# Optimization experiments

Measured on AMD Instinct MI355X. Metric: run time of the kernel, lower is better.

## Reference

```python
import jax, jax.numpy as jnp
import numpy as np

BOUND = 5.0
MIN_D = 1e-3
MIN_BW = 1e-3
MIN_BH = 1e-3
EPS = 1e-8
B, F, K = 131072, 256, 16


def setup_inputs() -> dict:
    key = jax.random.key(0)
    k1, k2, k3, k4 = jax.random.split(key, 4)
    return {
        "x": jax.random.normal(k1, (B, F), dtype=jnp.float32),
        "uw": jax.random.normal(k2, (F, K), dtype=jnp.float32),
        "uh": jax.random.normal(k3, (F, K), dtype=jnp.float32),
        "ud": jax.random.normal(k4, (F, K - 1), dtype=jnp.float32),
        "input_shift": jnp.zeros((F,), dtype=jnp.float32),
        "input_scale": jnp.ones((F,), dtype=jnp.float32),
    }


def _knots(u, mb):
    # u: [F, K] unnormalized bin sizes -> knot positions [F, K+1] and sizes [F, K]
    f, k = u.shape
    w = jax.nn.softmax(u, axis=-1)
    w = mb + (1.0 - mb * k) * w
    c = jnp.concatenate([jnp.zeros((f, 1), u.dtype), jnp.cumsum(w, axis=-1)], axis=-1)
    c = 2.0 * BOUND * c - BOUND
    c = c.at[:, 0].set(-BOUND).at[:, -1].set(BOUND)
    return c, c[:, 1:] - c[:, :-1]


def reference(x, uw, uh, ud, input_shift, input_scale):
    f, k = uw.shape
    # normalize input to spline domain
    xn = (x - input_shift[None, :]) / input_scale[None, :]

    # knot positions / bin sizes
    cw, w = _knots(uw, MIN_BW)   # [F, K+1], [F, K]
    ch, h = _knots(uh, MIN_BH)

    # derivatives at knots; boundaries padded so derivative = 1 (linear tails)
    const = float(np.log(np.expm1(1.0 - MIN_D)))
    pad = jnp.full((f, 1), const, dtype=ud.dtype)
    d = MIN_D + jax.nn.softplus(jnp.concatenate([pad, ud, pad], axis=-1))  # [F, K+1]

    inside = (xn > -BOUND) & (xn < BOUND)
    xc = jnp.clip(xn, -BOUND, BOUND)

    # per-feature bucketize: searchsorted over each feature's knots
    idx = jax.vmap(lambda a, v: jnp.searchsorted(a, v, side="right"),
                   in_axes=(0, 1), out_axes=1)(cw, xc) - 1  # [B, F]
    idx = jnp.clip(idx, 0, k - 1)

    fa = jnp.arange(f)[None, :]
    icw = cw[fa, idx]   # left knot x
    ibw = w[fa, idx]    # bin width
    ich = ch[fa, idx]   # left knot y
    ibh = h[fa, idx]    # bin height
    delta = ibh / ibw
    d0 = d[fa, idx]
    d1 = d[fa, idx + 1]

    # rational-quadratic evaluation
    theta = (xc - icw) / ibw
    t1m = theta * (1.0 - theta)
    numer = ibh * (delta * theta * theta + d0 * t1m)
    denom = delta + (d0 + d1 - 2.0 * delta) * t1m
    s = jnp.where(inside, ich + numer / denom, xn)  # identity linear tails

    # gauge fix: standardize per feature with batch stats (biased var)
    mean = jnp.mean(s, axis=0)
    var = jnp.mean((s - mean[None, :]) ** 2, axis=0)
    z = (s - mean[None, :]) / jnp.sqrt(var[None, :] + EPS)
    return z
```

## Files before the change

### kernel.cpp

```cpp
#include <hip/hip_runtime.h>
#include <math.h>


#define FEAT 256
#define KBINS 16
#define BATCH 131072
#define BOUNDF 5.0f
#define MIN_Df 1e-3f
#define MIN_BWf 1e-3f
#define MIN_BHf 1e-3f
#define EPSF 1e-8f

#define FT_TILES 4
#define FT 64
#define RB 256
#define ROWS_PB (BATCH / RB)
#define SLOTS 4
#define ITERS (ROWS_PB / SLOTS)

#define OFF_P0   0
#define OFF_P1   17408
#define OFF_CW   34816
#define OFF_MEAN 39168
#define OFF_ISTD 39424
#define OFF_PS   39680
#define OFF_PS2  (OFF_PS + 1024 * 64)

__global__ __launch_bounds__(256) void k_params(const float* __restrict__ uw,
                                                const float* __restrict__ uh,
                                                const float* __restrict__ ud,
                                                float* __restrict__ ws) {
    int f = threadIdx.x;
    float cw[17], ch[17], dv[17];
    {
        float u[KBINS];
#pragma unroll
        for (int j = 0; j < KBINS; j++) u[j] = uw[f * KBINS + j];
        float m = u[0];
#pragma unroll
        for (int j = 1; j < KBINS; j++) m = fmaxf(m, u[j]);
        float ssum = 0.f;
#pragma unroll
        for (int j = 0; j < KBINS; j++) { u[j] = expf(u[j] - m); ssum += u[j]; }
        float inv = 1.0f / ssum;
        float cum = 0.f;
        cw[0] = -BOUNDF;
#pragma unroll
        for (int j = 1; j < KBINS; j++) {
            float wj = MIN_BWf + (1.0f - MIN_BWf * (float)KBINS) * (u[j - 1] * inv);
            cum += wj;
            cw[j] = 2.0f * BOUNDF * cum - BOUNDF;
        }
        cw[KBINS] = BOUNDF;
    }
    {
        float u[KBINS];
#pragma unroll
        for (int j = 0; j < KBINS; j++) u[j] = uh[f * KBINS + j];
        float m = u[0];
#pragma unroll
        for (int j = 1; j < KBINS; j++) m = fmaxf(m, u[j]);
        float ssum = 0.f;
#pragma unroll
        for (int j = 0; j < KBINS; j++) { u[j] = expf(u[j] - m); ssum += u[j]; }
        float inv = 1.0f / ssum;
        float cum = 0.f;
        ch[0] = -BOUNDF;
#pragma unroll
        for (int j = 1; j < KBINS; j++) {
            float wj = MIN_BHf + (1.0f - MIN_BHf * (float)KBINS) * (u[j - 1] * inv);
            cum += wj;
            ch[j] = 2.0f * BOUNDF * cum - BOUNDF;
        }
        ch[KBINS] = BOUNDF;
    }
    {
        dv[0] = 1.0f;
        dv[KBINS] = 1.0f;
#pragma unroll
        for (int j = 1; j < KBINS; j++) {
            float v = ud[f * (KBINS - 1) + (j - 1)];
            float sp = fmaxf(v, 0.0f) + log1pf(expf(-fabsf(v)));
            dv[j] = MIN_Df + sp;
        }
    }
#pragma unroll
    for (int j = 0; j <= KBINS; j++) ws[OFF_CW + f * 17 + j] = cw[j];
    float4* P0g = (float4*)(ws + OFF_P0);
    float4* P1g = (float4*)(ws + OFF_P1);
#pragma unroll
    for (int i = 0; i < KBINS; i++) {
        float w = cw[i + 1] - cw[i];
        float binv = 1.0f / w;
        float hb = ch[i + 1] - ch[i];
        float delta = hb * binv;
        float4 p0, p1;
        p0.x = cw[i] * binv;
        p0.y = binv;
        p0.z = hb * delta;
        p0.w = hb * dv[i];
        p1.x = dv[i] + dv[i + 1] - 2.0f * delta;
        p1.y = delta;
        p1.z = ch[i];
        p1.w = 0.0f;
        P0g[f * 17 + i] = p0;
        P1g[f * 17 + i] = p1;
    }
}

__device__ __forceinline__ float eval_rq(float xv, float a, float nb,
                                         const float4* __restrict__ sP0,
                                         const float4* __restrict__ sP1,
                                         const float kn[15], int l17) {
    float xn = fmaf(xv, a, nb);
    float xc = fminf(fmaxf(xn, -BOUNDF), BOUNDF);
    int idx = 0;
#pragma unroll
    for (int j = 0; j < 15; j++) idx += (xc >= kn[j]) ? 1 : 0;
    int o = l17 + idx;
    float4 p0 = sP0[o];
    float4 p1 = sP1[o];
    float th = fmaf(xc, p0.y, -p0.x);
    float th2 = th * th;
    float t1m = th - th2;
    float numer = fmaf(p0.z, th2, p0.w * t1m);
    float denom = fmaf(p1.x, t1m, p1.y);
    float s = fmaf(numer, __builtin_amdgcn_rcpf(denom), p1.z);
    return (fabsf(xn) < BOUNDF) ? s : xn;
}

__global__ __launch_bounds__(256, 4) void k_pass1(const float* __restrict__ X,
                                                  const float* __restrict__ shiftp,
                                                  const float* __restrict__ scalep,
                                                  float* __restrict__ ws) {
    __shared__ float4 sP0[FT * 17];
    __shared__ float4 sP1[FT * 17];
    __shared__ float red[2][SLOTS][FT];
    int t = threadIdx.x;
    int rb = blockIdx.x, ft = blockIdx.y;
    const float4* P0g = (const float4*)(ws + OFF_P0) + ft * FT * 17;
    const float4* P1g = (const float4*)(ws + OFF_P1) + ft * FT * 17;
    for (int i = t; i < FT * 17; i += 256) { sP0[i] = P0g[i]; sP1[i] = P1g[i]; }
    int l = t & 63, slot = t >> 6;
    int f = ft * FT + l;
    float kn[15];
#pragma unroll
    for (int j = 0; j < 15; j++) kn[j] = ws[OFF_CW + f * 17 + 1 + j];
    float a = 1.0f / scalep[f];
    float nb = -shiftp[f] * a;
    int l17 = l * 17;
    __syncthreads();
    const float* Xp = X + (size_t)(rb * ROWS_PB + slot) * FEAT + f;
    float sum = 0.f, sumsq = 0.f;
    for (int r = 0; r < ITERS; r += 4) {
        float x0 = Xp[0 * SLOTS * FEAT];
        float x1 = Xp[1 * SLOTS * FEAT];
        float x2 = Xp[2 * SLOTS * FEAT];
        float x3 = Xp[3 * SLOTS * FEAT];
        Xp += 4 * SLOTS * FEAT;
        float s0 = eval_rq(x0, a, nb, sP0, sP1, kn, l17);
        float s1 = eval_rq(x1, a, nb, sP0, sP1, kn, l17);
        float s2 = eval_rq(x2, a, nb, sP0, sP1, kn, l17);
        float s3 = eval_rq(x3, a, nb, sP0, sP1, kn, l17);
        sum += s0; sumsq = fmaf(s0, s0, sumsq);
        sum += s1; sumsq = fmaf(s1, s1, sumsq);
        sum += s2; sumsq = fmaf(s2, s2, sumsq);
        sum += s3; sumsq = fmaf(s3, s3, sumsq);
    }
    red[0][slot][l] = sum;
    red[1][slot][l] = sumsq;
    __syncthreads();
    if (t < FT) {
        float v = red[0][0][t] + red[0][1][t] + red[0][2][t] + red[0][3][t];
        ws[OFF_PS + (ft * RB + rb) * FT + t] = v;
    } else if (t < 2 * FT) {
        int u = t - FT;
        float v = red[1][0][u] + red[1][1][u] + red[1][2][u] + red[1][3][u];
        ws[OFF_PS2 + (ft * RB + rb) * FT + u] = v;
    }
}

__global__ __launch_bounds__(256) void k_reduce(float* __restrict__ ws) {
    int f = blockIdx.x;
    int ft = f >> 6, l = f & 63;
    int t = threadIdx.x;
    __shared__ float r1[256], r2[256];
    r1[t] = ws[OFF_PS + (ft * RB + t) * FT + l];
    r2[t] = ws[OFF_PS2 + (ft * RB + t) * FT + l];
    __syncthreads();
    for (int off = 128; off > 0; off >>= 1) {
        if (t < off) { r1[t] += r1[t + off]; r2[t] += r2[t + off]; }
        __syncthreads();
    }
    if (t == 0) {
        float mean = r1[0] * (1.0f / (float)BATCH);
        float var = r2[0] * (1.0f / (float)BATCH) - mean * mean;
        var = fmaxf(var, 0.0f);
        ws[OFF_MEAN + f] = mean;
        ws[OFF_ISTD + f] = 1.0f / sqrtf(var + EPSF);
    }
}

__global__ __launch_bounds__(256, 4) void k_pass2(const float* __restrict__ X,
                                                  const float* __restrict__ shiftp,
                                                  const float* __restrict__ scalep,
                                                  const float* __restrict__ ws,
                                                  float* __restrict__ Z) {
    __shared__ float4 sP0[FT * 17];
    __shared__ float4 sP1[FT * 17];
    int t = threadIdx.x;
    int rb = blockIdx.x, ft = blockIdx.y;
    const float4* P0g = (const float4*)(ws + OFF_P0) + ft * FT * 17;
    const float4* P1g = (const float4*)(ws + OFF_P1) + ft * FT * 17;
    for (int i = t; i < FT * 17; i += 256) { sP0[i] = P0g[i]; sP1[i] = P1g[i]; }
    int l = t & 63, slot = t >> 6;
    int f = ft * FT + l;
    float kn[15];
#pragma unroll
    for (int j = 0; j < 15; j++) kn[j] = ws[OFF_CW + f * 17 + 1 + j];
    float a = 1.0f / scalep[f];
    float nb = -shiftp[f] * a;
    float mean = ws[OFF_MEAN + f];
    float istd = ws[OFF_ISTD + f];
    int l17 = l * 17;
    __syncthreads();
    size_t base = (size_t)(rb * ROWS_PB + slot) * FEAT + f;
    const float* Xp = X + base;
    float* Zp = Z + base;
    for (int r = 0; r < ITERS; r += 4) {
        float x0 = Xp[0 * SLOTS * FEAT];
        float x1 = Xp[1 * SLOTS * FEAT];
        float x2 = Xp[2 * SLOTS * FEAT];
        float x3 = Xp[3 * SLOTS * FEAT];
        Xp += 4 * SLOTS * FEAT;
        float s0 = eval_rq(x0, a, nb, sP0, sP1, kn, l17);
        float s1 = eval_rq(x1, a, nb, sP0, sP1, kn, l17);
        float s2 = eval_rq(x2, a, nb, sP0, sP1, kn, l17);
        float s3 = eval_rq(x3, a, nb, sP0, sP1, kn, l17);
        Zp[0 * SLOTS * FEAT] = (s0 - mean) * istd;
        Zp[1 * SLOTS * FEAT] = (s1 - mean) * istd;
        Zp[2 * SLOTS * FEAT] = (s2 - mean) * istd;
        Zp[3 * SLOTS * FEAT] = (s3 - mean) * istd;
        Zp += 4 * SLOTS * FEAT;
    }
}

extern "C" void kernel_launch(void* const* d_in, const int* in_sizes, int n_in,
                              void* d_out, int out_size, void* d_ws, size_t ws_size,
                              hipStream_t stream) {
    const float* x     = (const float*)d_in[0];
    const float* uw    = (const float*)d_in[1];
    const float* uh    = (const float*)d_in[2];
    const float* ud    = (const float*)d_in[3];
    const float* shift = (const float*)d_in[4];
    const float* scale = (const float*)d_in[5];
    float* out = (float*)d_out;
    float* ws  = (float*)d_ws;

    k_params<<<1, 256, 0, stream>>>(uw, uh, ud, ws);
    k_pass1<<<dim3(RB, FT_TILES), 256, 0, stream>>>(x, shift, scale, ws);
    k_reduce<<<FEAT, 256, 0, stream>>>(ws);
    k_pass2<<<dim3(RB, FT_TILES), 256, 0, stream>>>(x, shift, scale, ws, out);
}
```

Before: 116.8 us.

## Cache spline output as bf16 in pass 1 and stream-normalize in pass 2

Pass 1 now writes the spline output as bf16 into workspace, and a new vectorized pass 2 reads it back and applies the per-feature normalization, replacing the re-read of x and re-evaluation of the spline. Feature tiles shrink to 32 with 8 row slots, and occupancy hints are raised. Total memory traffic stays about the same, but pass 2 drops the searchsorted and rational-quadratic math. This relies on enough workspace (falling back to the old path otherwise) and adds bf16 rounding error to the output.

```diff
diff --git a/kernel.cpp b/kernel.cpp
--- a/kernel.cpp
+++ b/kernel.cpp
@@ -11,25 +11,34 @@
 #define MIN_BHf 1e-3f
 #define EPSF 1e-8f
 
-#define FT_TILES 4
-#define FT 64
-#define RB 256
-#define ROWS_PB (BATCH / RB)
-#define SLOTS 4
-#define ITERS (ROWS_PB / SLOTS)
-
-#define OFF_P0   0
-#define OFF_P1   17408
-#define OFF_CW   34816
-#define OFF_MEAN 39168
-#define OFF_ISTD 39424
-#define OFF_PS   39680
-#define OFF_PS2  (OFF_PS + 1024 * 64)
+#define FTB 32
+#define FT_TILES 8
+#define SLOTB 8
+#define RBB 256
+#define ROWS_PB (BATCH / RBB)
+#define ITERB (ROWS_PB / SLOTB)
+
+#define R_P0   0
+#define R_P1   17408
+#define R_CW   34816
+#define R_MEAN 39168
+#define R_ISTD 39424
+#define R_PS   39680
+#define R_PS2  (R_PS + 2048 * 32)
+#define TAB_FLOATS (R_PS2 + 2048 * 32)
+#define S_ELEMS ((size_t)BATCH * FEAT)
+#define S_FLOATS (S_ELEMS / 2)
+
+__device__ __forceinline__ unsigned short f2bf(float x) {
+    unsigned int b = __float_as_uint(x);
+    unsigned int r = (b + 0x7fffu + ((b >> 16) & 1u)) >> 16;
+    return (unsigned short)r;
+}
 
 __global__ __launch_bounds__(256) void k_params(const float* __restrict__ uw,
                                                 const float* __restrict__ uh,
                                                 const float* __restrict__ ud,
-                                                float* __restrict__ ws) {
+                                                float* __restrict__ tab) {
     int f = threadIdx.x;
     float cw[17], ch[17], dv[17];
     {
@@ -85,9 +94,9 @@
         }
     }
 #pragma unroll
-    for (int j = 0; j <= KBINS; j++) ws[OFF_CW + f * 17 + j] = cw[j];
-    float4* P0g = (float4*)(ws + OFF_P0);
-    float4* P1g = (float4*)(ws + OFF_P1);
+    for (int j = 0; j <= KBINS; j++) tab[R_CW + f * 17 + j] = cw[j];
+    float4* P0g = (float4*)(tab + R_P0);
+    float4* P1g = (float4*)(tab + R_P1);
 #pragma unroll
     for (int i = 0; i < KBINS; i++) {
         float w = cw[i + 1] - cw[i];
@@ -129,39 +138,50 @@
     return (fabsf(xn) < BOUNDF) ? s : xn;
 }
 
-__global__ __launch_bounds__(256, 4) void k_pass1(const float* __restrict__ X,
+template <bool STORE_S>
+__global__ __launch_bounds__(256, 6) void k_pass1(const float* __restrict__ X,
                                                   const float* __restrict__ shiftp,
                                                   const float* __restrict__ scalep,
-                                                  float* __restrict__ ws) {
-    __shared__ float4 sP0[FT * 17];
-    __shared__ float4 sP1[FT * 17];
-    __shared__ float red[2][SLOTS][FT];
+                                                  float* __restrict__ tab,
+                                                  unsigned short* __restrict__ S) {
+    __shared__ float4 sP0[FTB * 17];
+    __shared__ float4 sP1[FTB * 17];
+    __shared__ float red[2][SLOTB][FTB];
     int t = threadIdx.x;
     int rb = blockIdx.x, ft = blockIdx.y;
-    const float4* P0g = (const float4*)(ws + OFF_P0) + ft * FT * 17;
-    const float4* P1g = (const float4*)(ws + OFF_P1) + ft * FT * 17;
-    for (int i = t; i < FT * 17; i += 256) { sP0[i] = P0g[i]; sP1[i] = P1g[i]; }
-    int l = t & 63, slot = t >> 6;
-    int f = ft * FT + l;
+    const float4* P0g = (const float4*)(tab + R_P0) + ft * FTB * 17;
+    const float4* P1g = (const float4*)(tab + R_P1) + ft * FTB * 17;
+    for (int i = t; i < FTB * 17; i += 256) { sP0[i] = P0g[i]; sP1[i] = P1g[i]; }
+    int l = t & 31, slot = t >> 5;
+    int f = ft * FTB + l;
     float kn[15];
 #pragma unroll
-    for (int j = 0; j < 15; j++) kn[j] = ws[OFF_CW + f * 17 + 1 + j];
+    for (int j = 0; j < 15; j++) kn[j] = tab[R_CW + f * 17 + 1 + j];
     float a = 1.0f / scalep[f];
     float nb = -shiftp[f] * a;
     int l17 = l * 17;
     __syncthreads();
-    const float* Xp = X + (size_t)(rb * ROWS_PB + slot) * FEAT + f;
+    size_t base = (size_t)(rb * ROWS_PB + slot) * FEAT + f;
+    const float* Xp = X + base;
+    unsigned short* Sp = STORE_S ? (S + base) : nullptr;
     float sum = 0.f, sumsq = 0.f;
-    for (int r = 0; r < ITERS; r += 4) {
-        float x0 = Xp[0 * SLOTS * FEAT];
-        float x1 = Xp[1 * SLOTS * FEAT];
-        float x2 = Xp[2 * SLOTS * FEAT];
-        float x3 = Xp[3 * SLOTS * FEAT];
-        Xp += 4 * SLOTS * FEAT;
+    for (int r = 0; r < ITERB; r += 4) {
+        float x0 = Xp[0 * SLOTB * FEAT];
+        float x1 = Xp[1 * SLOTB * FEAT];
+        float x2 = Xp[2 * SLOTB * FEAT];
+        float x3 = Xp[3 * SLOTB * FEAT];
+        Xp += 4 * SLOTB * FEAT;
         float s0 = eval_rq(x0, a, nb, sP0, sP1, kn, l17);
         float s1 = eval_rq(x1, a, nb, sP0, sP1, kn, l17);
         float s2 = eval_rq(x2, a, nb, sP0, sP1, kn, l17);
         float s3 = eval_rq(x3, a, nb, sP0, sP1, kn, l17);
+        if (STORE_S) {
+            Sp[0 * SLOTB * FEAT] = f2bf(s0);
+            Sp[1 * SLOTB * FEAT] = f2bf(s1);
+            Sp[2 * SLOTB * FEAT] = f2bf(s2);
+            Sp[3 * SLOTB * FEAT] = f2bf(s3);
+            Sp += 4 * SLOTB * FEAT;
+        }
         sum += s0; sumsq = fmaf(s0, s0, sumsq);
         sum += s1; sumsq = fmaf(s1, s1, sumsq);
         sum += s2; sumsq = fmaf(s2, s2, sumsq);
@@ -170,23 +190,27 @@
     red[0][slot][l] = sum;
     red[1][slot][l] = sumsq;
     __syncthreads();
-    if (t < FT) {
-        float v = red[0][0][t] + red[0][1][t] + red[0][2][t] + red[0][3][t];
-        ws[OFF_PS + (ft * RB + rb) * FT + t] = v;
-    } else if (t < 2 * FT) {
-        int u = t - FT;
-        float v = red[1][0][u] + red[1][1][u] + red[1][2][u] + red[1][3][u];
-        ws[OFF_PS2 + (ft * RB + rb) * FT + u] = v;
-    }
-}
-
-__global__ __launch_bounds__(256) void k_reduce(float* __restrict__ ws) {
+    if (t < FTB) {
+        float v = 0.f;
+#pragma unroll
+        for (int s2i = 0; s2i < SLOTB; s2i++) v += red[0][s2i][t];
+        tab[R_PS + (ft * RBB + rb) * FTB + t] = v;
+    } else if (t < 2 * FTB) {
+        int u = t - FTB;
+        float v = 0.f;
+#pragma unroll
+        for (int s2i = 0; s2i < SLOTB; s2i++) v += red[1][s2i][u];
+        tab[R_PS2 + (ft * RBB + rb) * FTB + u] = v;
+    }
+}
+
+__global__ __launch_bounds__(256) void k_reduce(float* __restrict__ tab) {
     int f = blockIdx.x;
-    int ft = f >> 6, l = f & 63;
+    int ft = f >> 5, l = f & 31;
     int t = threadIdx.x;
     __shared__ float r1[256], r2[256];
-    r1[t] = ws[OFF_PS + (ft * RB + t) * FT + l];
-    r2[t] = ws[OFF_PS2 + (ft * RB + t) * FT + l];
+    r1[t] = tab[R_PS + (ft * RBB + t) * FTB + l];
+    r2[t] = tab[R_PS2 + (ft * RBB + t) * FTB + l];
     __syncthreads();
     for (int off = 128; off > 0; off >>= 1) {
         if (t < off) { r1[t] += r1[t + off]; r2[t] += r2[t + off]; }
@@ -196,52 +220,87 @@
         float mean = r1[0] * (1.0f / (float)BATCH);
         float var = r2[0] * (1.0f / (float)BATCH) - mean * mean;
         var = fmaxf(var, 0.0f);
-        ws[OFF_MEAN + f] = mean;
-        ws[OFF_ISTD + f] = 1.0f / sqrtf(var + EPSF);
-    }
-}
-
-__global__ __launch_bounds__(256, 4) void k_pass2(const float* __restrict__ X,
-                                                  const float* __restrict__ shiftp,
-                                                  const float* __restrict__ scalep,
-                                                  const float* __restrict__ ws,
-                                                  float* __restrict__ Z) {
-    __shared__ float4 sP0[FT * 17];
-    __shared__ float4 sP1[FT * 17];
+        tab[R_MEAN + f] = mean;
+        tab[R_ISTD + f] = 1.0f / sqrtf(var + EPSF);
+    }
+}
+
+__global__ __launch_bounds__(256, 8) void k_pass2_stream(const unsigned short* __restrict__ S,
+                                                         const float* __restrict__ tab,
+                                                         float* __restrict__ Z) {
+    int gid = blockIdx.x * 256 + threadIdx.x;
+    int fg = gid & 31;
+    int rs = gid >> 5;
+    const float* meanp = tab + R_MEAN + fg * 8;
+    const float* istdp = tab + R_ISTD + fg * 8;
+    float istd[8], nmi[8];
+#pragma unroll
+    for (int j = 0; j < 8; j++) {
+        float m = meanp[j];
+        float is = istdp[j];
+        istd[j] = is;
+        nmi[j] = -m * is;
+    }
+    size_t idx = (size_t)rs * 8 * FEAT + fg * 8;
+#pragma unroll
+    for (int r = 0; r < 8; r++) {
+        uint4 sv = *(const uint4*)(S + idx);
+        float z0 = fmaf(__uint_as_float((sv.x & 0xffffu) << 16), istd[0], nmi[0]);
+        float z1 = fmaf(__uint_as_float(sv.x & 0xffff0000u),     istd[1], nmi[1]);
+        float z2 = fmaf(__uint_as_float((sv.y & 0xffffu) << 16), istd[2], nmi[2]);
+        float z3 = fmaf(__uint_as_float(sv.y & 0xffff0000u),     istd[3], nmi[3]);
+        float z4 = fmaf(__uint_as_float((sv.z & 0xffffu) << 16), istd[4], nmi[4]);
+        float z5 = fmaf(__uint_as_float(sv.z & 0xffff0000u),     istd[5], nmi[5]);
+        float z6 = fmaf(__uint_as_float((sv.w & 0xffffu) << 16), istd[6], nmi[6]);
+        float z7 = fmaf(__uint_as_float(sv.w & 0xffff0000u),     istd[7], nmi[7]);
+        float4* Zp = (float4*)(Z + idx);
+        Zp[0] = make_float4(z0, z1, z2, z3);
+        Zp[1] = make_float4(z4, z5, z6, z7);
+        idx += FEAT;
+    }
+}
+
+__global__ __launch_bounds__(256, 6) void k_pass2_eval(const float* __restrict__ X,
+                                                       const float* __restrict__ shiftp,
+                                                       const float* __restrict__ scalep,
+                                                       const float* __restrict__ tab,
+                                                       float* __restrict__ Z) {
+    __shared__ float4 sP0[FTB * 17];
+    __shared__ float4 sP1[FTB * 17];
     int t = threadIdx.x;
     int rb = blockIdx.x, ft = blockIdx.y;
-    const float4* P0g = (const float4*)(ws + OFF_P0) + ft * FT * 17;
-    const float4* P1g = (const float4*)(ws + OFF_P1) + ft * FT * 17;
-    for (int i = t; i < FT * 17; i += 256) { sP0[i] = P0g[i]; sP1[i] = P1g[i]; }
-    int l = t & 63, slot = t >> 6;
-    int f = ft * FT + l;
+    const float4* P0g = (const float4*)(tab + R_P0) + ft * FTB * 17;
+    const float4* P1g = (const float4*)(tab + R_P1) + ft * FTB * 17;
+    for (int i = t; i < FTB * 17; i += 256) { sP0[i] = P0g[i]; sP1[i] = P1g[i]; }
+    int l = t & 31, slot = t >> 5;
+    int f = ft * FTB + l;
     float kn[15];
 #pragma unroll
-    for (int j = 0; j < 15; j++) kn[j] = ws[OFF_CW + f * 17 + 1 + j];
+    for (int j = 0; j < 15; j++) kn[j] = tab[R_CW + f * 17 + 1 + j];
     float a = 1.0f / scalep[f];
     float nb = -shiftp[f] * a;
-    float mean = ws[OFF_MEAN + f];
-    float istd = ws[OFF_ISTD + f];
+    float mean = tab[R_MEAN + f];
+    float istd = tab[R_ISTD + f];
     int l17 = l * 17;
     __syncthreads();
     size_t base = (size_t)(rb * ROWS_PB + slot) * FEAT + f;
     const float* Xp = X + base;
     float* Zp = Z + base;
-    for (int r = 0; r < ITERS; r += 4) {
-        float x0 = Xp[0 * SLOTS * FEAT];
-        float x1 = Xp[1 * SLOTS * FEAT];
-        float x2 = Xp[2 * SLOTS * FEAT];
-        float x3 = Xp[3 * SLOTS * FEAT];
-        Xp += 4 * SLOTS * FEAT;
+    for (int r = 0; r < ITERB; r += 4) {
+        float x0 = Xp[0 * SLOTB * FEAT];
+        float x1 = Xp[1 * SLOTB * FEAT];
+        float x2 = Xp[2 * SLOTB * FEAT];
+        float x3 = Xp[3 * SLOTB * FEAT];
+        Xp += 4 * SLOTB * FEAT;
         float s0 = eval_rq(x0, a, nb, sP0, sP1, kn, l17);
         float s1 = eval_rq(x1, a, nb, sP0, sP1, kn, l17);
         float s2 = eval_rq(x2, a, nb, sP0, sP1, kn, l17);
         float s3 = eval_rq(x3, a, nb, sP0, sP1, kn, l17);
-        Zp[0 * SLOTS * FEAT] = (s0 - mean) * istd;
-        Zp[1 * SLOTS * FEAT] = (s1 - mean) * istd;
-        Zp[2 * SLOTS * FEAT] = (s2 - mean) * istd;
-        Zp[3 * SLOTS * FEAT] = (s3 - mean) * istd;
-        Zp += 4 * SLOTS * FEAT;
+        Zp[0 * SLOTB * FEAT] = (s0 - mean) * istd;
+        Zp[1 * SLOTB * FEAT] = (s1 - mean) * istd;
+        Zp[2 * SLOTB * FEAT] = (s2 - mean) * istd;
+        Zp[3 * SLOTB * FEAT] = (s3 - mean) * istd;
+        Zp += 4 * SLOTB * FEAT;
     }
 }
 
@@ -257,8 +316,19 @@
     float* out = (float*)d_out;
     float* ws  = (float*)d_ws;
 
-    k_params<<<1, 256, 0, stream>>>(uw, uh, ud, ws);
-    k_pass1<<<dim3(RB, FT_TILES), 256, 0, stream>>>(x, shift, scale, ws);
-    k_reduce<<<FEAT, 256, 0, stream>>>(ws);
-    k_pass2<<<dim3(RB, FT_TILES), 256, 0, stream>>>(x, shift, scale, ws, out);
-}
+    size_t need = (S_FLOATS + (size_t)TAB_FLOATS) * sizeof(float);
+    bool useS = ws_size >= need;
+    float* tab = ws + (useS ? S_FLOATS : 0);
+    unsigned short* S = (unsigned short*)ws;
+
+    k_params<<<1, 256, 0, stream>>>(uw, uh, ud, tab);
+    if (useS) {
+        k_pass1<true><<<dim3(RBB, FT_TILES), 256, 0, stream>>>(x, shift, scale, tab, S);
+        k_reduce<<<FEAT, 256, 0, stream>>>(tab);
+        k_pass2_stream<<<2048, 256, 0, stream>>>(S, tab, out);
+    } else {
+        k_pass1<false><<<dim3(RBB, FT_TILES), 256, 0, stream>>>(x, shift, scale, tab, nullptr);
+        k_reduce<<<FEAT, 256, 0, stream>>>(tab);
+        k_pass2_eval<<<dim3(RBB, FT_TILES), 256, 0, stream>>>(x, shift, scale, tab, out);
+    }
+}
```

Result: faster. 114.3 us (-2.2%).
